# Optimization experiments

Measured on AMD Instinct MI355X. Metric: run time of the kernel, lower is better.

## Reference

```python
import jax, jax.numpy as jnp
from jax import lax
import numpy as np

B, C_IN, H, W = 32, 128, 64, 64
C_OUT, K, KH, KW = 256, 4, 3, 3
HIDDEN = C_IN  # in_planes != 3 -> hidden_planes = in_planes
T_TEMP = 34.0
BN_EPS = 1e-5


def setup_inputs() -> dict:
    key = jax.random.key(0)
    ks = jax.random.split(key, 4)
    return {
        "x": jax.random.normal(ks[0], (B, C_IN, H, W), dtype=jnp.float32),
        "w_fc1": jax.random.normal(ks[1], (HIDDEN, C_IN), dtype=jnp.float32) * (2.0 / C_IN) ** 0.5,
        "bn1_gamma": jnp.ones((HIDDEN,), jnp.float32),
        "bn1_beta": jnp.zeros((HIDDEN,), jnp.float32),
        "bn1_mean": jnp.zeros((HIDDEN,), jnp.float32),
        "bn1_var": jnp.ones((HIDDEN,), jnp.float32),
        "w_fc2": jax.random.normal(ks[2], (K * C_IN, HIDDEN), dtype=jnp.float32) * (2.0 / HIDDEN) ** 0.5,
        "b_fc2": jnp.zeros((K * C_IN,), jnp.float32),
        "bn2_gamma": jnp.ones((K * C_IN,), jnp.float32),
        "bn2_beta": jnp.zeros((K * C_IN,), jnp.float32),
        "bn2_mean": jnp.zeros((K * C_IN,), jnp.float32),
        "bn2_var": jnp.ones((K * C_IN,), jnp.float32),
        "anchored_w": jax.random.normal(ks[3], (K, C_OUT, C_IN, KH, KW), dtype=jnp.float32) * (2.0 / (C_OUT * KH * KW)) ** 0.5,
        "anchored_b": jnp.zeros((K, C_OUT), jnp.float32),
    }


def _bn(v, gamma, beta, mean, var):
    return (v - mean) * gamma * lax.rsqrt(var + BN_EPS) + beta


def reference(x, w_fc1, bn1_gamma, bn1_beta, bn1_mean, bn1_var,
              w_fc2, b_fc2, bn2_gamma, bn2_beta, bn2_mean, bn2_var,
              anchored_w, anchored_b):
    # ----- CFG routing: squeeze-excite style softmax over K*C_in -----
    pooled = x.mean(axis=(2, 3))                      # [B, C_in]  (adaptive avg pool to 1x1)
    h = pooled @ w_fc1.T                              # [B, hidden] (1x1 conv, no bias)
    h = jax.nn.relu(_bn(h, bn1_gamma, bn1_beta, bn1_mean, bn1_var))
    t = h @ w_fc2.T + b_fc2                           # [B, K*C_in]
    t = _bn(t, bn2_gamma, bn2_beta, bn2_mean, bn2_var)
    theta = jax.nn.softmax(t / T_TEMP, axis=1)        # [B, K*C_in]
    theta_r = theta.reshape(-1, K, anchored_w.shape[2])  # [B, K, C_in]

    # ----- per-sample kernel mixture: sum_k theta[b,k,i] * W[k,o,i,h,w] -----
    w = jnp.einsum('bki,koihw->boihw', theta_r, anchored_w)  # [B, C_out, C_in, KH, KW]
    b = theta_r.mean(axis=2) @ anchored_b                    # [B, C_out]

    # ----- per-sample conv (equiv. to grouped conv with groups=B) -----
    def conv1(xi, wi):
        return lax.conv_general_dilated(
            xi[None], wi, window_strides=(1, 1), padding=((1, 1), (1, 1)),
            dimension_numbers=('NCHW', 'OIHW', 'NCHW'))[0]

    out = jax.vmap(conv1)(x, w) + b[:, :, None, None]  # [B, C_out, H, W]
    return out
```

## Files before the change

### kernel.cpp

```cpp
#include <hip/hip_runtime.h>

typedef __attribute__((ext_vector_type(8))) __bf16 bf16x8;
typedef __attribute__((ext_vector_type(4))) float f32x4;

__device__ __forceinline__ unsigned short f2bf(float f) {
  unsigned u = __builtin_bit_cast(unsigned, f);
  u = (u + 0x7fffu + ((u >> 16) & 1u)) >> 16;
  return (unsigned short)u;
}

__device__ __forceinline__ void gload_lds16(const void* g, void* l) {
  __builtin_amdgcn_global_load_lds(
      (const __attribute__((address_space(1))) unsigned int*)g,
      (__attribute__((address_space(3))) unsigned int*)l, 16, 0, 0);
}

__global__ __launch_bounds__(256) void k_pool_convert(
    const float* __restrict__ x, float* __restrict__ psum,
    unsigned short* __restrict__ xbf) {
  __shared__ float xs[128][65];
  const int b = blockIdx.x >> 6;
  const int y = blockIdx.x & 63;
  const int t = threadIdx.x;
  const float* src = x + ((size_t)b * 128) * 4096 + y * 64;
#pragma unroll
  for (int i = 0; i < 8; ++i) {
    int idx = t + i * 256;
    int c = idx >> 4, x4 = (idx & 15) << 2;
    float4 v = *(const float4*)(src + (size_t)c * 4096 + x4);
    xs[c][x4] = v.x; xs[c][x4 + 1] = v.y; xs[c][x4 + 2] = v.z; xs[c][x4 + 3] = v.w;
  }
  __syncthreads();
  if (t < 128) {
    float s = 0.f;
#pragma unroll
    for (int j = 0; j < 64; ++j) s += xs[t][j];
    psum[((size_t)b * 128 + t) * 64 + y] = s;
  }
#pragma unroll
  for (int i = 0; i < 4; ++i) {
    int idx = t + i * 256;
    int q = idx & 3, xx = (idx >> 2) & 63, g = idx >> 8;
    unsigned wd[4];
#pragma unroll
    for (int j = 0; j < 4; ++j) {
      unsigned lo = f2bf(xs[g * 32 + q * 8 + 2 * j][xx]);
      unsigned hi = f2bf(xs[g * 32 + q * 8 + 2 * j + 1][xx]);
      wd[j] = lo | (hi << 16);
    }
    *(uint4*)(xbf + ((((size_t)b * 4 + g) * 4096) + y * 64 + xx) * 32 + q * 8) =
        make_uint4(wd[0], wd[1], wd[2], wd[3]);
  }
}

__global__ __launch_bounds__(128) void k_route(
    const float* __restrict__ psum, const float* __restrict__ w_fc1,
    const float* __restrict__ g1, const float* __restrict__ be1,
    const float* __restrict__ m1, const float* __restrict__ v1,
    const float* __restrict__ w_fc2, const float* __restrict__ bfc2,
    const float* __restrict__ g2, const float* __restrict__ be2,
    const float* __restrict__ m2, const float* __restrict__ v2,
    const float* __restrict__ ab, float* __restrict__ theta,
    float* __restrict__ bias) {
  __shared__ float pooled[128], hs[128], red[128], tkm[4];
  const int b = blockIdx.x, t = threadIdx.x;
  float s = 0.f;
  const float* ps = psum + ((size_t)b * 128 + t) * 64;
  for (int j = 0; j < 64; ++j) s += ps[j];
  pooled[t] = s * (1.0f / 4096.0f);
  __syncthreads();
  float acc = 0.f;
  const float* w1r = w_fc1 + t * 128;
  for (int i = 0; i < 128; ++i) acc += pooled[i] * w1r[i];
  acc = (acc - m1[t]) * g1[t] * rsqrtf(v1[t] + 1e-5f) + be1[t];
  hs[t] = fmaxf(acc, 0.f);
  __syncthreads();
  float tv[4];
  for (int q = 0; q < 4; ++q) {
    int m = q * 128 + t;
    const float* w2r = w_fc2 + (size_t)m * 128;
    float a2 = bfc2[m];
    for (int i = 0; i < 128; ++i) a2 += hs[i] * w2r[i];
    a2 = (a2 - m2[m]) * g2[m] * rsqrtf(v2[m] + 1e-5f) + be2[m];
    tv[q] = a2 * (1.0f / 34.0f);
  }
  float mx = fmaxf(fmaxf(tv[0], tv[1]), fmaxf(tv[2], tv[3]));
  red[t] = mx; __syncthreads();
  for (int o = 64; o > 0; o >>= 1) { if (t < o) red[t] = fmaxf(red[t], red[t + o]); __syncthreads(); }
  mx = red[0]; __syncthreads();
  float e[4], ssum = 0.f;
  for (int q = 0; q < 4; ++q) { e[q] = expf(tv[q] - mx); ssum += e[q]; }
  red[t] = ssum; __syncthreads();
  for (int o = 64; o > 0; o >>= 1) { if (t < o) red[t] += red[t + o]; __syncthreads(); }
  float inv = 1.0f / red[0]; __syncthreads();
  float th[4];
  for (int q = 0; q < 4; ++q) { th[q] = e[q] * inv; theta[b * 512 + q * 128 + t] = th[q]; }
  for (int q = 0; q < 4; ++q) {
    red[t] = th[q]; __syncthreads();
    for (int o = 64; o > 0; o >>= 1) { if (t < o) red[t] += red[t + o]; __syncthreads(); }
    if (t == 0) tkm[q] = red[0] * (1.0f / 128.0f);
    __syncthreads();
  }
  for (int o = t; o < 256; o += 128) {
    float bb = 0.f;
    for (int k = 0; k < 4; ++k) bb += tkm[k] * ab[k * 256 + o];
    bias[b * 256 + o] = bb;
  }
}

__global__ __launch_bounds__(256) void k_mix(
    const float* __restrict__ aw, const float* __restrict__ theta,
    unsigned short* __restrict__ wmix) {
  __shared__ float aw_s[4][32][33];
  __shared__ float th_s[32][4][32];
  const int bx = blockIdx.x;
  const int oq = bx & 3, obl = (bx >> 2) & 1, ks = bx >> 3;
  const int g = ks / 9, tt = ks % 9;
  const int tid = threadIdx.x;
#pragma unroll
  for (int i = 0; i < 16; ++i) {
    int e = tid + i * 256;
    int i32 = e & 31, o32 = (e >> 5) & 31, k = e >> 10;
    aw_s[k][i32][o32] =
        aw[((size_t)((k * 256 + obl * 128 + oq * 32 + o32) * 128) + g * 32 + i32) * 9 + tt];
    int kb = (e >> 5) & 3, bb = e >> 7;
    th_s[bb][kb][i32] = theta[bb * 512 + kb * 128 + g * 32 + i32];
  }
  __syncthreads();
  for (int it = 0; it < 16; ++it) {
    int b = it * 2 + (tid >> 7);
    int u = tid & 127;
    int o32 = u >> 2, q = u & 3;
    unsigned wd[4];
#pragma unroll
    for (int jj = 0; jj < 4; ++jj) {
      int i0 = q * 8 + jj * 2, i1 = i0 + 1;
      float v0 = th_s[b][0][i0] * aw_s[0][i0][o32] + th_s[b][1][i0] * aw_s[1][i0][o32]
               + th_s[b][2][i0] * aw_s[2][i0][o32] + th_s[b][3][i0] * aw_s[3][i0][o32];
      float v1 = th_s[b][0][i1] * aw_s[0][i1][o32] + th_s[b][1][i1] * aw_s[1][i1][o32]
               + th_s[b][2][i1] * aw_s[2][i1][o32] + th_s[b][3][i1] * aw_s[3][i1][o32];
      wd[jj] = (unsigned)f2bf(v0) | ((unsigned)f2bf(v1) << 16);
    }
    unsigned A = (unsigned)(((oq * 32 + o32) * 32 + q * 8) * 2);
    unsigned P = A ^ ((A >> 2) & 0x70u);
    size_t tilebase = (((size_t)b * 36 + ks) * 2 + obl) * 8192;
    *(uint4*)((char*)wmix + tilebase + P) = make_uint4(wd[0], wd[1], wd[2], wd[3]);
  }
}

__global__ __launch_bounds__(256, 3) void k_conv(
    const unsigned short* __restrict__ xbf, const unsigned short* __restrict__ wmix,
    const float* __restrict__ bias, float* __restrict__ out) {
  __shared__ __align__(16) char xls[21120];
  __shared__ __align__(16) char wls[3][8192];
  const int bx = blockIdx.x;
  const int wgid = ((bx & 7) << 8) | (bx >> 3);
  const int b = wgid >> 6, obl = (wgid >> 5) & 1, pblk = wgid & 31;
  const int tid = threadIdx.x;
  const int lane = tid & 63, wv = tid >> 6;
  const int ow = wv >> 1, pw = wv & 1;
  const int y0 = pblk << 1;
  const int l15 = lane & 15, l4 = lane >> 4;

  unsigned a_off0 = ((unsigned)(l15 * 64 + l4 * 16)) ^ ((unsigned)(l15 & 7) << 4);
  a_off0 += (unsigned)(ow * 4096);

  f32x4 acc[4][4] = {};

  const unsigned short* xsrc_b = xbf + (size_t)b * 4 * 4096 * 32;

  auto stageW = [&](int ks, int buf) {
    const unsigned short* wsrc = wmix + ((size_t)(b * 36 + ks) * 2 + obl) * 4096;
#pragma unroll
    for (int p = 0; p < 2; ++p)
      gload_lds16((const char*)wsrc + p * 4096 + wv * 1024 + lane * 16,
                  wls[buf] + p * 4096 + wv * 1024);
  };

  uint4 xr[5];
  auto loadX = [&](int g) {
    const unsigned short* xsrc = xsrc_b + (size_t)g * (4096 * 32);
#pragma unroll
    for (int i = 0; i < 4; ++i) {
      int e = tid + i * 256;
      int q = e & 3, rc = e >> 2, c = rc % 66, r = rc / 66;
      int yy = y0 - 1 + r, xx = c - 1;
      uint4 v = make_uint4(0u, 0u, 0u, 0u);
      if ((unsigned)yy < 64u && (unsigned)xx < 64u)
        v = *(const uint4*)(xsrc + (((size_t)yy << 6) + xx) * 32 + q * 8);
      xr[i] = v;
    }
    if (tid < 32) {
      int e = tid + 1024;
      int q = e & 3, rc = e >> 2, c = rc % 66, r = rc / 66;
      int yy = y0 - 1 + r, xx = c - 1;
      uint4 v = make_uint4(0u, 0u, 0u, 0u);
      if ((unsigned)yy < 64u && (unsigned)xx < 64u)
        v = *(const uint4*)(xsrc + (((size_t)yy << 6) + xx) * 32 + q * 8);
      xr[4] = v;
    }
  };
  auto writeX = [&]() {
#pragma unroll
    for (int i = 0; i < 4; ++i) {
      int e = tid + i * 256;
      int q = e & 3, rc = e >> 2, c = rc % 66, r = rc / 66;
      *(uint4*)(xls + (r * 66 + c) * 80 + q * 16) = xr[i];
    }
    if (tid < 32) {
      int e = tid + 1024;
      int q = e & 3, rc = e >> 2, c = rc % 66, r = rc / 66;
      *(uint4*)(xls + (r * 66 + c) * 80 + q * 16) = xr[4];
    }
  };

  loadX(0);
  writeX();
  stageW(0, 0);
  stageW(1, 1);
  asm volatile("s_waitcnt lgkmcnt(0)" ::: "memory");

#pragma unroll
  for (int ks = 0; ks < 36; ++ks) {
    if (ks == 35) asm volatile("s_waitcnt vmcnt(0)" ::: "memory");
    else          asm volatile("s_waitcnt vmcnt(2)" ::: "memory");
    __builtin_amdgcn_s_barrier();
    asm volatile("" ::: "memory");
    if (ks > 0 && ks % 9 == 0) {
      writeX();
      asm volatile("s_waitcnt lgkmcnt(0)" ::: "memory");
      __builtin_amdgcn_s_barrier();
      asm volatile("" ::: "memory");
    }
    if (ks % 9 == 8 && ks < 35) {
      loadX(ks / 9 + 1);
      asm volatile("" ::: "memory");
    }
    if (ks + 2 < 36) stageW(ks + 2, (ks + 2) % 3);
    const int dy = (ks % 9) / 3, dx = (ks % 9) % 3;
    bf16x8 bfr[4], afr[4];
    const char* bbase = xls + ((pw + dy) * 66 + dx + l15) * 80 + l4 * 16;
#pragma unroll
    for (int pf = 0; pf < 4; ++pf) bfr[pf] = *(const bf16x8*)(bbase + pf * 1280);
    const char* abase = wls[ks % 3] + a_off0;
#pragma unroll
    for (int of = 0; of < 4; ++of) afr[of] = *(const bf16x8*)(abase + of * 1024);
    __builtin_amdgcn_s_setprio(1);
#pragma unroll
    for (int of = 0; of < 4; ++of)
#pragma unroll
      for (int pf = 0; pf < 4; ++pf)
        acc[of][pf] = __builtin_amdgcn_mfma_f32_16x16x32_bf16(afr[of], bfr[pf], acc[of][pf], 0, 0, 0);
    __builtin_amdgcn_s_setprio(0);
  }

  const float* bp = bias + b * 256 + obl * 128 + ow * 64;
  float bv[4][4];
#pragma unroll
  for (int of = 0; of < 4; ++of)
#pragma unroll
    for (int j = 0; j < 4; ++j) bv[of][j] = bp[of * 16 + l4 * 4 + j];
  size_t outbase = ((size_t)(b * 256 + obl * 128 + ow * 64)) * 4096 + pblk * 128 + pw * 64;
#pragma unroll
  for (int of = 0; of < 4; ++of)
#pragma unroll
    for (int pf = 0; pf < 4; ++pf)
#pragma unroll
      for (int j = 0; j < 4; ++j)
        out[outbase + (size_t)(of * 16 + l4 * 4 + j) * 4096 + pf * 16 + l15] =
            acc[of][pf][j] + bv[of][j];
}

extern "C" void kernel_launch(void* const* d_in, const int* in_sizes, int n_in,
                              void* d_out, int out_size, void* d_ws, size_t ws_size,
                              hipStream_t stream) {
  const float* x     = (const float*)d_in[0];
  const float* w_fc1 = (const float*)d_in[1];
  const float* g1    = (const float*)d_in[2];
  const float* be1   = (const float*)d_in[3];
  const float* m1    = (const float*)d_in[4];
  const float* v1    = (const float*)d_in[5];
  const float* w_fc2 = (const float*)d_in[6];
  const float* bfc2  = (const float*)d_in[7];
  const float* g2    = (const float*)d_in[8];
  const float* be2   = (const float*)d_in[9];
  const float* m2    = (const float*)d_in[10];
  const float* v2    = (const float*)d_in[11];
  const float* aw    = (const float*)d_in[12];
  const float* ab    = (const float*)d_in[13];
  float* out = (float*)d_out;

  char* ws = (char*)d_ws;
  unsigned short* xbf  = (unsigned short*)(ws);
  unsigned short* wmix = (unsigned short*)(ws + 33554432);
  float* psum  = (float*)(ws + 52428800);
  float* theta = (float*)(ws + 53477376);
  float* bias  = (float*)(ws + 53542912);

  hipLaunchKernelGGL(k_pool_convert, dim3(2048), dim3(256), 0, stream, x, psum, xbf);
  hipLaunchKernelGGL(k_route, dim3(32), dim3(128), 0, stream, psum, w_fc1, g1, be1, m1, v1,
                     w_fc2, bfc2, g2, be2, m2, v2, ab, theta, bias);
  hipLaunchKernelGGL(k_mix, dim3(288), dim3(256), 0, stream, aw, theta, wmix);
  hipLaunchKernelGGL(k_conv, dim3(2048), dim3(256), 0, stream, xbf, wmix, bias, out);
}
```

Baseline: 140.8 us.

## Enlarge conv tile to all 256 output channels per block with double-buffered weights

Each conv workgroup now computes all 256 output channels for a two-row pixel tile instead of 128. Each wave covers 64 channels by 128 pixels with twice as many accumulators, so the staged input halo is reused across both output-channel halves and the grid is halved. Weight staging drops from triple buffering with two steps of lookahead to double buffering with one step and a full vmcnt(0) wait. This raises register pressure, lowering the occupancy target to 2 blocks per SM, and exposes more global-load latency.

```diff
diff --git a/kernel.cpp b/kernel.cpp
--- a/kernel.cpp
+++ b/kernel.cpp
@@ -148,32 +148,31 @@
   }
 }
 
-__global__ __launch_bounds__(256, 3) void k_conv(
+__global__ __launch_bounds__(256, 2) void k_conv(
     const unsigned short* __restrict__ xbf, const unsigned short* __restrict__ wmix,
     const float* __restrict__ bias, float* __restrict__ out) {
   __shared__ __align__(16) char xls[21120];
-  __shared__ __align__(16) char wls[3][8192];
+  __shared__ __align__(16) char wls[2][16384];
   const int bx = blockIdx.x;
-  const int wgid = ((bx & 7) << 8) | (bx >> 3);
-  const int b = wgid >> 6, obl = (wgid >> 5) & 1, pblk = wgid & 31;
+  const int wgid = ((bx & 7) << 7) | (bx >> 3);
+  const int b = wgid >> 5, pblk = wgid & 31;
   const int tid = threadIdx.x;
   const int lane = tid & 63, wv = tid >> 6;
-  const int ow = wv >> 1, pw = wv & 1;
   const int y0 = pblk << 1;
   const int l15 = lane & 15, l4 = lane >> 4;
 
   unsigned a_off0 = ((unsigned)(l15 * 64 + l4 * 16)) ^ ((unsigned)(l15 & 7) << 4);
-  a_off0 += (unsigned)(ow * 4096);
-
-  f32x4 acc[4][4] = {};
+  a_off0 += (unsigned)(wv * 4096);
+
+  f32x4 acc[4][8] = {};
 
   const unsigned short* xsrc_b = xbf + (size_t)b * 4 * 4096 * 32;
 
   auto stageW = [&](int ks, int buf) {
-    const unsigned short* wsrc = wmix + ((size_t)(b * 36 + ks) * 2 + obl) * 4096;
-#pragma unroll
-    for (int p = 0; p < 2; ++p)
-      gload_lds16((const char*)wsrc + p * 4096 + wv * 1024 + lane * 16,
+    const char* wsrc = (const char*)wmix + (size_t)(b * 36 + ks) * 16384;
+#pragma unroll
+    for (int p = 0; p < 4; ++p)
+      gload_lds16(wsrc + p * 4096 + wv * 1024 + lane * 16,
                   wls[buf] + p * 4096 + wv * 1024);
   };
 
@@ -217,13 +216,11 @@
   loadX(0);
   writeX();
   stageW(0, 0);
-  stageW(1, 1);
   asm volatile("s_waitcnt lgkmcnt(0)" ::: "memory");
 
 #pragma unroll
   for (int ks = 0; ks < 36; ++ks) {
-    if (ks == 35) asm volatile("s_waitcnt vmcnt(0)" ::: "memory");
-    else          asm volatile("s_waitcnt vmcnt(2)" ::: "memory");
+    asm volatile("s_waitcnt vmcnt(0)" ::: "memory");
     __builtin_amdgcn_s_barrier();
     asm volatile("" ::: "memory");
     if (ks > 0 && ks % 9 == 0) {
@@ -236,39 +233,43 @@
       loadX(ks / 9 + 1);
       asm volatile("" ::: "memory");
     }
-    if (ks + 2 < 36) stageW(ks + 2, (ks + 2) % 3);
+    if (ks + 1 < 36) stageW(ks + 1, (ks + 1) & 1);
     const int dy = (ks % 9) / 3, dx = (ks % 9) % 3;
-    bf16x8 bfr[4], afr[4];
-    const char* bbase = xls + ((pw + dy) * 66 + dx + l15) * 80 + l4 * 16;
+    bf16x8 bfr[8], afr[4];
+    const char* bbase = xls + ((0 + dy) * 66 + dx + l15) * 80 + l4 * 16;
 #pragma unroll
     for (int pf = 0; pf < 4; ++pf) bfr[pf] = *(const bf16x8*)(bbase + pf * 1280);
-    const char* abase = wls[ks % 3] + a_off0;
+#pragma unroll
+    for (int pf = 0; pf < 4; ++pf) bfr[pf + 4] = *(const bf16x8*)(bbase + 5280 + pf * 1280);
+    const char* abase = wls[ks & 1] + a_off0;
 #pragma unroll
     for (int of = 0; of < 4; ++of) afr[of] = *(const bf16x8*)(abase + of * 1024);
     __builtin_amdgcn_s_setprio(1);
 #pragma unroll
     for (int of = 0; of < 4; ++of)
 #pragma unroll
-      for (int pf = 0; pf < 4; ++pf)
+      for (int pf = 0; pf < 8; ++pf)
         acc[of][pf] = __builtin_amdgcn_mfma_f32_16x16x32_bf16(afr[of], bfr[pf], acc[of][pf], 0, 0, 0);
     __builtin_amdgcn_s_setprio(0);
   }
 
-  const float* bp = bias + b * 256 + obl * 128 + ow * 64;
+  const float* bp = bias + b * 256 + wv * 64;
   float bv[4][4];
 #pragma unroll
   for (int of = 0; of < 4; ++of)
 #pragma unroll
     for (int j = 0; j < 4; ++j) bv[of][j] = bp[of * 16 + l4 * 4 + j];
-  size_t outbase = ((size_t)(b * 256 + obl * 128 + ow * 64)) * 4096 + pblk * 128 + pw * 64;
+  size_t outbase = ((size_t)(b * 256 + wv * 64)) * 4096 + (size_t)y0 * 64;
 #pragma unroll
   for (int of = 0; of < 4; ++of)
 #pragma unroll
-    for (int pf = 0; pf < 4; ++pf)
+    for (int pf = 0; pf < 8; ++pf) {
+      int py = pf >> 2, px0 = (pf & 3) * 16;
 #pragma unroll
       for (int j = 0; j < 4; ++j)
-        out[outbase + (size_t)(of * 16 + l4 * 4 + j) * 4096 + pf * 16 + l15] =
+        out[outbase + (size_t)(of * 16 + l4 * 4 + j) * 4096 + py * 64 + px0 + l15] =
             acc[of][pf][j] + bv[of][j];
+    }
 }
 
 extern "C" void kernel_launch(void* const* d_in, const int* in_sizes, int n_in,
@@ -301,5 +302,5 @@
   hipLaunchKernelGGL(k_route, dim3(32), dim3(128), 0, stream, psum, w_fc1, g1, be1, m1, v1,
                      w_fc2, bfc2, g2, be2, m2, v2, ab, theta, bias);
   hipLaunchKernelGGL(k_mix, dim3(288), dim3(256), 0, stream, aw, theta, wmix);
-  hipLaunchKernelGGL(k_conv, dim3(2048), dim3(256), 0, stream, xbf, wmix, bias, out);
-}
+  hipLaunchKernelGGL(k_conv, dim3(1024), dim3(256), 0, stream, xbf, wmix, bias, out);
+}
```

New measurement: 132.6 us. 1.06x faster.
